# Kernel optimization log

Hardware: AMD Instinct MI355X
Metric: run time of the kernel (lower is better)

## Reference

```python
import jax, jax.numpy as jnp
import numpy as np

EPS = 1e-8  # torch F.cosine_similarity default eps
NEG = -1e9  # masked_fill value


def setup_inputs() -> dict:
    key = jax.random.key(0)
    k1, k2, k3 = jax.random.split(key, 3)
    B, Sq, Sk, D = 4, 2048, 2048, 1024
    query = jax.random.normal(k1, (B, Sq, 1, D), dtype=jnp.float32)
    key_t = jax.random.normal(k2, (B, 1, Sk, D), dtype=jnp.float32)
    mask = jax.random.randint(k3, (B, Sk), 0, 2, dtype=jnp.int32)
    return {"query": query, "key": key_t, "mask": mask}


def reference(query, key, mask):
    # query: [B, Sq, 1, D], key: [B, 1, Sk, D]
    q = query[:, :, 0, :]  # [B, Sq, D]
    k = key[:, 0, :, :]    # [B, Sk, D]
    # cosine_similarity(q, k, dim=3) = (q.k) / (max(|q|,eps) * max(|k|,eps))
    qn = jnp.maximum(jnp.linalg.norm(q, axis=-1), EPS)  # [B, Sq]
    kn = jnp.maximum(jnp.linalg.norm(k, axis=-1), EPS)  # [B, Sk]
    dot = jnp.einsum('bqd,bkd->bqk', q, k)              # [B, Sq, Sk]
    scores = dot / (qn[:, :, None] * kn[:, None, :])
    # mask.unsqueeze(1).repeat(1, Sq, 1) -> broadcast [B, 1, Sk] over Sq
    scores = jnp.where(mask[:, None, :] == 0, NEG, scores)
    return scores
```

## Files before the change

kernel.cpp:

```cpp
#include <hip/hip_runtime.h>
#include <hip/hip_bf16.h>
#include <stdint.h>


constexpr int B_  = 4;
constexpr int SQ  = 2048;
constexpr int SK  = 2048;
constexpr int D_  = 1024;
constexpr int BM  = 128;
constexpr int BN  = 128;
constexpr int BK  = 64;
constexpr int BKf = 32;

typedef __attribute__((ext_vector_type(8))) short    short8;
typedef __attribute__((ext_vector_type(4))) float    f32x4;
typedef __attribute__((ext_vector_type(4))) unsigned uint4v;
typedef unsigned int u32;

__device__ inline unsigned pack_bf16(float lo, float hi) {
  union { float f; unsigned u; } a, b;
  a.f = lo; b.f = hi;
  return __builtin_amdgcn_perm(b.u, a.u, 0x07060302u);
}

__device__ inline void async_ld16(const void* g, void* l) {
  __builtin_amdgcn_global_load_lds((const __attribute__((address_space(1))) u32*)g,
                                   (__attribute__((address_space(3))) u32*)l, 16, 0, 0);
}

constexpr int ROWS_Q = B_ * SQ;
constexpr int ROWS_T = B_ * (SQ + SK);

__global__ __launch_bounds__(256) void convert_norm(
    const float* __restrict__ Q, const float* __restrict__ Km,
    unsigned short* __restrict__ Qb, unsigned short* __restrict__ Kb,
    float* __restrict__ invQ, float* __restrict__ invK)
{
  const int row  = blockIdx.x * 4 + (threadIdx.x >> 6);
  const int lane = threadIdx.x & 63;

  const float* src; unsigned short* dst; float* inv;
  if (row < ROWS_Q) {
    src = Q  + (size_t)row * D_;
    dst = Qb + (size_t)row * D_;
    inv = invQ + row;
  } else {
    int r = row - ROWS_Q;
    src = Km + (size_t)r * D_;
    dst = Kb + (size_t)r * D_;
    inv = invK + r;
  }

  const f32x4* s4 = (const f32x4*)(src + lane * 16);
  f32x4 v[4];
  #pragma unroll
  for (int i = 0; i < 4; ++i) v[i] = s4[i];

  float ss = 0.0f;
  unsigned p[8];
  #pragma unroll
  for (int i = 0; i < 4; ++i) {
    p[2*i]   = pack_bf16(v[i].x, v[i].y);
    p[2*i+1] = pack_bf16(v[i].z, v[i].w);
    ss += v[i].x*v[i].x + v[i].y*v[i].y + v[i].z*v[i].z + v[i].w*v[i].w;
  }
  uint4v w0 = {p[0], p[1], p[2], p[3]};
  uint4v w1 = {p[4], p[5], p[6], p[7]};
  uint4v* d4 = (uint4v*)(dst + lane * 16);
  d4[0] = w0; d4[1] = w1;

  #pragma unroll
  for (int off = 32; off > 0; off >>= 1) ss += __shfl_xor(ss, off);
  if (lane == 0) *inv = 1.0f / fmaxf(sqrtf(ss), 1e-8f);
}

__global__ __launch_bounds__(256, 2) void ca_gemm_bf(
    const unsigned short* __restrict__ Qb,
    const unsigned short* __restrict__ Kb,
    const float* __restrict__ invQ,
    const float* __restrict__ invK,
    const int*   __restrict__ mask,
    float*       __restrict__ out)
{
  __shared__ __align__(16) unsigned short As[BM * BK];
  __shared__ __align__(16) unsigned short Bs[BN * BK];

  const int tid  = threadIdx.x;
  const int lane = tid & 63;
  const int w    = tid >> 6;
  const int b    = blockIdx.z;
  const int tm0  = blockIdx.y * BM;
  const int tn0  = blockIdx.x * BN;

  const int srow   = lane >> 3;
  const int gchunk = (lane & 7) ^ srow;

  const char* qrow = (const char*)(Qb + ((size_t)b * SQ + tm0 + w * 32 + srow) * D_) + gchunk * 16;
  const char* krow = (const char*)(Kb + ((size_t)b * SK + tn0 + w * 32 + srow) * D_) + gchunk * 16;
  const size_t rstep8 = (size_t)8 * D_ * 2;

  unsigned short* ldsA = &As[(size_t)(w * 32) * BK];
  unsigned short* ldsB = &Bs[(size_t)(w * 32) * BK];

  f32x4 zero4 = {0.0f, 0.0f, 0.0f, 0.0f};
  f32x4 acc[4][4];
  #pragma unroll
  for (int i = 0; i < 4; ++i)
    #pragma unroll
    for (int j = 0; j < 4; ++j) acc[i][j] = zero4;

  const int wm = (w >> 1) * 64;
  const int wn = (w & 1) * 64;
  const int lr = lane & 15;
  const int lq = lane >> 4;

  for (int k0 = 0; k0 < D_; k0 += BK) {
    __syncthreads();
    const size_t kb = (size_t)k0 * 2;
    #pragma unroll
    for (int i = 0; i < 4; ++i)
      async_ld16(qrow + kb + i * rstep8, ldsA + i * 8 * BK);
    #pragma unroll
    for (int i = 0; i < 4; ++i)
      async_ld16(krow + kb + i * rstep8, ldsB + i * 8 * BK);
    __syncthreads();

    #pragma unroll
    for (int s = 0; s < 2; ++s) {
      short8 af[4], bf[4];
      #pragma unroll
      for (int t = 0; t < 4; ++t) {
        const int r = wm + t * 16 + lr;
        af[t] = *(const short8*)&As[(size_t)r * BK + (size_t)(((s * 4 + lq) ^ (r & 7)) * 8)];
      }
      #pragma unroll
      for (int t = 0; t < 4; ++t) {
        const int r = wn + t * 16 + lr;
        bf[t] = *(const short8*)&Bs[(size_t)r * BK + (size_t)(((s * 4 + lq) ^ (r & 7)) * 8)];
      }
      #pragma unroll
      for (int i = 0; i < 4; ++i)
        #pragma unroll
        for (int j = 0; j < 4; ++j)
          acc[i][j] = __builtin_amdgcn_mfma_f32_16x16x32_bf16(af[i], bf[j], acc[i][j], 0, 0, 0);
    }
  }

  #pragma unroll
  for (int tn = 0; tn < 4; ++tn) {
    const int gc = tn0 + wn + tn * 16 + lr;
    const int mk = mask[b * SK + gc];
    const float ib = invK[b * SK + gc];
    #pragma unroll
    for (int tm = 0; tm < 4; ++tm) {
      const int lrow = wm + tm * 16 + lq * 4;
      #pragma unroll
      for (int r = 0; r < 4; ++r) {
        const float ia = invQ[b * SQ + tm0 + lrow + r];
        float v = mk ? acc[tm][tn][r] * ia * ib : -1000000000.0f;
        out[((size_t)b * SQ + tm0 + lrow + r) * SK + gc] = v;
      }
    }
  }
}

constexpr int LDK = 40;

__global__ __launch_bounds__(256, 2) void ca_gemm(
    const float* __restrict__ Q, const float* __restrict__ Km,
    const int* __restrict__ mask, float* __restrict__ out)
{
  __shared__ __align__(16) short As[BM * LDK];
  __shared__ __align__(16) short Bs[BN * LDK];
  __shared__ float ssA_part[256];
  __shared__ float ssB_part[256];
  __shared__ float invA[BM];
  __shared__ float invB[BN];

  const int tid  = threadIdx.x;
  const int lane = tid & 63;
  const int w    = tid >> 6;
  const int b    = blockIdx.z;
  const int tm0  = blockIdx.y * BM;
  const int tn0  = blockIdx.x * BN;

  const int ra = tid >> 1;
  const int ka = (tid & 1) * 16;

  const float* qp = Q  + ((size_t)b * SQ + tm0 + ra) * D_ + ka;
  const float* kp = Km + ((size_t)b * SK + tn0 + ra) * D_ + ka;

  f32x4 zero4 = {0.0f, 0.0f, 0.0f, 0.0f};
  f32x4 acc[4][4];
  #pragma unroll
  for (int i = 0; i < 4; ++i)
    #pragma unroll
    for (int j = 0; j < 4; ++j) acc[i][j] = zero4;

  float ssA = 0.0f, ssB = 0.0f;

  const int wm = (w >> 1) * 64;
  const int wn = (w & 1) * 64;
  const int lr = lane & 15;
  const int lq = lane >> 4;

  short* aw = &As[ra * LDK + ka];
  short* bw = &Bs[ra * LDK + ka];

  for (int k0 = 0; k0 < D_; k0 += BKf) {
    f32x4 av[4], bv[4];
    #pragma unroll
    for (int i = 0; i < 4; ++i) av[i] = *(const f32x4*)(qp + 4 * i);
    #pragma unroll
    for (int i = 0; i < 4; ++i) bv[i] = *(const f32x4*)(kp + 4 * i);
    qp += BKf; kp += BKf;

    unsigned pa[8], pb[8];
    #pragma unroll
    for (int i = 0; i < 4; ++i) {
      pa[2*i]   = pack_bf16(av[i].x, av[i].y);
      pa[2*i+1] = pack_bf16(av[i].z, av[i].w);
      pb[2*i]   = pack_bf16(bv[i].x, bv[i].y);
      pb[2*i+1] = pack_bf16(bv[i].z, bv[i].w);
      ssA += av[i].x*av[i].x + av[i].y*av[i].y + av[i].z*av[i].z + av[i].w*av[i].w;
      ssB += bv[i].x*bv[i].x + bv[i].y*bv[i].y + bv[i].z*bv[i].z + bv[i].w*bv[i].w;
    }

    __syncthreads();
    {
      uint4v wa0 = {pa[0], pa[1], pa[2], pa[3]};
      uint4v wa1 = {pa[4], pa[5], pa[6], pa[7]};
      uint4v wb0 = {pb[0], pb[1], pb[2], pb[3]};
      uint4v wb1 = {pb[4], pb[5], pb[6], pb[7]};
      *(uint4v*)(aw)     = wa0;
      *(uint4v*)(aw + 8) = wa1;
      *(uint4v*)(bw)     = wb0;
      *(uint4v*)(bw + 8) = wb1;
    }
    __syncthreads();

    short8 af[4], bf[4];
    #pragma unroll
    for (int t = 0; t < 4; ++t)
      af[t] = *(const short8*)&As[(wm + t * 16 + lr) * LDK + lq * 8];
    #pragma unroll
    for (int t = 0; t < 4; ++t)
      bf[t] = *(const short8*)&Bs[(wn + t * 16 + lr) * LDK + lq * 8];

    #pragma unroll
    for (int i = 0; i < 4; ++i)
      #pragma unroll
      for (int j = 0; j < 4; ++j)
        acc[i][j] = __builtin_amdgcn_mfma_f32_16x16x32_bf16(af[i], bf[j], acc[i][j], 0, 0, 0);
  }

  ssA_part[tid] = ssA;
  ssB_part[tid] = ssB;
  __syncthreads();
  if (tid < BM) {
    float s = ssA_part[2 * tid] + ssA_part[2 * tid + 1];
    invA[tid] = 1.0f / fmaxf(sqrtf(s), 1e-8f);
  } else {
    int r = tid - BM;
    float s = ssB_part[2 * r] + ssB_part[2 * r + 1];
    invB[r] = 1.0f / fmaxf(sqrtf(s), 1e-8f);
  }
  __syncthreads();

  #pragma unroll
  for (int tn = 0; tn < 4; ++tn) {
    const int lc = wn + tn * 16 + lr;
    const int gc = tn0 + lc;
    const int mk = mask[b * SK + gc];
    const float ib = invB[lc];
    #pragma unroll
    for (int tm = 0; tm < 4; ++tm) {
      const int lrow = wm + tm * 16 + lq * 4;
      #pragma unroll
      for (int r = 0; r < 4; ++r) {
        float v = mk ? acc[tm][tn][r] * invA[lrow + r] * ib : -1000000000.0f;
        out[((size_t)b * SQ + tm0 + lrow + r) * SK + gc] = v;
      }
    }
  }
}

extern "C" void kernel_launch(void* const* d_in, const int* in_sizes, int n_in,
                              void* d_out, int out_size, void* d_ws, size_t ws_size,
                              hipStream_t stream) {
  const float* Q    = (const float*)d_in[0];
  const float* Km   = (const float*)d_in[1];
  const int*   mask = (const int*)d_in[2];
  float*       out  = (float*)d_out;

  const size_t nQ   = (size_t)B_ * SQ * D_;
  const size_t nK   = (size_t)B_ * SK * D_;
  const size_t need = (nQ + nK) * 2 + (size_t)B_ * (SQ + SK) * 4;
  if (ws_size >= need) {
    unsigned short* Qb = (unsigned short*)d_ws;
    unsigned short* Kb = Qb + nQ;
    float*          iQ = (float*)(Kb + nK);
    float*          iK = iQ + (size_t)B_ * SQ;
    convert_norm<<<ROWS_T / 4, 256, 0, stream>>>(Q, Km, Qb, Kb, iQ, iK);
    dim3 grid(SK / BN, SQ / BM, B_);
    ca_gemm_bf<<<grid, dim3(256), 0, stream>>>(Qb, Kb, iQ, iK, mask, out);
  } else {
    dim3 grid(SK / BN, SQ / BM, B_);
    ca_gemm<<<grid, dim3(256), 0, stream>>>(Q, Km, mask, out);
  }
}
```

Measured before the change: 161.7 us.

## Double-buffer LDS tiles in bf16 GEMM with async prefetch and nontemporal stores

After: 169.9 us. 5.0% more time.

```diff
diff --git a/kernel.cpp b/kernel.cpp
--- a/kernel.cpp
+++ b/kernel.cpp
@@ -9,8 +9,8 @@
 constexpr int D_  = 1024;
 constexpr int BM  = 128;
 constexpr int BN  = 128;
-constexpr int BK  = 64;
-constexpr int BKf = 32;
+constexpr int BK  = 32;
+constexpr int NIT = D_ / BK;
 
 typedef __attribute__((ext_vector_type(8))) short    short8;
 typedef __attribute__((ext_vector_type(4))) float    f32x4;
@@ -82,8 +82,8 @@
     const int*   __restrict__ mask,
     float*       __restrict__ out)
 {
-  __shared__ __align__(16) unsigned short As[BM * BK];
-  __shared__ __align__(16) unsigned short Bs[BN * BK];
+  __shared__ __align__(16) unsigned short As[2][BM * BK];
+  __shared__ __align__(16) unsigned short Bs[2][BN * BK];
 
   const int tid  = threadIdx.x;
   const int lane = tid & 63;
@@ -92,15 +92,15 @@
   const int tm0  = blockIdx.y * BM;
   const int tn0  = blockIdx.x * BN;
 
-  const int srow   = lane >> 3;
-  const int gchunk = (lane & 7) ^ srow;
+  const int srow   = lane >> 2;
+  const int gchunk = (lane & 3) ^ ((lane >> 3) & 3);
 
   const char* qrow = (const char*)(Qb + ((size_t)b * SQ + tm0 + w * 32 + srow) * D_) + gchunk * 16;
   const char* krow = (const char*)(Kb + ((size_t)b * SK + tn0 + w * 32 + srow) * D_) + gchunk * 16;
-  const size_t rstep8 = (size_t)8 * D_ * 2;
-
-  unsigned short* ldsA = &As[(size_t)(w * 32) * BK];
-  unsigned short* ldsB = &Bs[(size_t)(w * 32) * BK];
+  const size_t rstep16 = (size_t)16 * D_ * 2;
+
+  unsigned short* ldsA0[2] = { &As[0][(w * 32) * BK], &As[1][(w * 32) * BK] };
+  unsigned short* ldsB0[2] = { &Bs[0][(w * 32) * BK], &Bs[1][(w * 32) * BK] };
 
   f32x4 zero4 = {0.0f, 0.0f, 0.0f, 0.0f};
   f32x4 acc[4][4];
@@ -114,51 +114,67 @@
   const int lr = lane & 15;
   const int lq = lane >> 4;
 
-  for (int k0 = 0; k0 < D_; k0 += BK) {
-    __syncthreads();
-    const size_t kb = (size_t)k0 * 2;
-    #pragma unroll
-    for (int i = 0; i < 4; ++i)
-      async_ld16(qrow + kb + i * rstep8, ldsA + i * 8 * BK);
-    #pragma unroll
-    for (int i = 0; i < 4; ++i)
-      async_ld16(krow + kb + i * rstep8, ldsB + i * 8 * BK);
-    __syncthreads();
-
-    #pragma unroll
-    for (int s = 0; s < 2; ++s) {
-      short8 af[4], bf[4];
-      #pragma unroll
-      for (int t = 0; t < 4; ++t) {
-        const int r = wm + t * 16 + lr;
-        af[t] = *(const short8*)&As[(size_t)r * BK + (size_t)(((s * 4 + lq) ^ (r & 7)) * 8)];
-      }
-      #pragma unroll
-      for (int t = 0; t < 4; ++t) {
-        const int r = wn + t * 16 + lr;
-        bf[t] = *(const short8*)&Bs[(size_t)r * BK + (size_t)(((s * 4 + lq) ^ (r & 7)) * 8)];
-      }
-      #pragma unroll
-      for (int i = 0; i < 4; ++i)
-        #pragma unroll
-        for (int j = 0; j < 4; ++j)
-          acc[i][j] = __builtin_amdgcn_mfma_f32_16x16x32_bf16(af[i], bf[j], acc[i][j], 0, 0, 0);
-    }
-  }
-
+  int   mk[4]; float ib[4]; float ia[4][4];
   #pragma unroll
   for (int tn = 0; tn < 4; ++tn) {
     const int gc = tn0 + wn + tn * 16 + lr;
-    const int mk = mask[b * SK + gc];
-    const float ib = invK[b * SK + gc];
+    mk[tn] = mask[b * SK + gc];
+    ib[tn] = invK[b * SK + gc];
+  }
+  #pragma unroll
+  for (int tm = 0; tm < 4; ++tm) {
+    const int lrow = wm + tm * 16 + lq * 4;
+    #pragma unroll
+    for (int r = 0; r < 4; ++r) ia[tm][r] = invQ[b * SQ + tm0 + lrow + r];
+  }
+
+  auto stage = [&](int buf, int k0) {
+    const size_t kb = (size_t)k0 * 2;
+    async_ld16(qrow + kb,           ldsA0[buf]);
+    async_ld16(qrow + kb + rstep16, ldsA0[buf] + 16 * BK);
+    async_ld16(krow + kb,           ldsB0[buf]);
+    async_ld16(krow + kb + rstep16, ldsB0[buf] + 16 * BK);
+  };
+
+  auto compute = [&](const unsigned short* Ac, const unsigned short* Bc) {
+    short8 af[4], bf[4];
+    #pragma unroll
+    for (int t = 0; t < 4; ++t) {
+      const int r = wm + t * 16 + lr;
+      af[t] = *(const short8*)&Ac[(size_t)r * BK + (size_t)((lq ^ ((r >> 1) & 3)) * 8)];
+    }
+    #pragma unroll
+    for (int t = 0; t < 4; ++t) {
+      const int r = wn + t * 16 + lr;
+      bf[t] = *(const short8*)&Bc[(size_t)r * BK + (size_t)((lq ^ ((r >> 1) & 3)) * 8)];
+    }
+    #pragma unroll
+    for (int i = 0; i < 4; ++i)
+      #pragma unroll
+      for (int j = 0; j < 4; ++j)
+        acc[i][j] = __builtin_amdgcn_mfma_f32_16x16x32_bf16(af[i], bf[j], acc[i][j], 0, 0, 0);
+  };
+
+  stage(0, 0);
+  for (int it = 0; it < NIT; it += 2) {
+    __syncthreads();
+    if (it + 1 < NIT) stage(1, (it + 1) * BK);
+    compute(As[0], Bs[0]);
+    __syncthreads();
+    if (it + 2 < NIT) stage(0, (it + 2) * BK);
+    compute(As[1], Bs[1]);
+  }
+
+  #pragma unroll
+  for (int tn = 0; tn < 4; ++tn) {
+    const int gc = tn0 + wn + tn * 16 + lr;
     #pragma unroll
     for (int tm = 0; tm < 4; ++tm) {
       const int lrow = wm + tm * 16 + lq * 4;
       #pragma unroll
       for (int r = 0; r < 4; ++r) {
-        const float ia = invQ[b * SQ + tm0 + lrow + r];
-        float v = mk ? acc[tm][tn][r] * ia * ib : -1000000000.0f;
-        out[((size_t)b * SQ + tm0 + lrow + r) * SK + gc] = v;
+        float v = mk[tn] ? acc[tm][tn][r] * ia[tm][r] * ib[tn] : -1000000000.0f;
+        __builtin_nontemporal_store(v, &out[((size_t)b * SQ + tm0 + lrow + r) * SK + gc]);
       }
     }
   }
@@ -207,13 +223,13 @@
   short* aw = &As[ra * LDK + ka];
   short* bw = &Bs[ra * LDK + ka];
 
-  for (int k0 = 0; k0 < D_; k0 += BKf) {
+  for (int k0 = 0; k0 < D_; k0 += 32) {
     f32x4 av[4], bv[4];
     #pragma unroll
     for (int i = 0; i < 4; ++i) av[i] = *(const f32x4*)(qp + 4 * i);
     #pragma unroll
     for (int i = 0; i < 4; ++i) bv[i] = *(const f32x4*)(kp + 4 * i);
-    qp += BKf; kp += BKf;
+    qp += 32; kp += 32;
 
     unsigned pa[8], pb[8];
     #pragma unroll
@@ -272,13 +288,13 @@
     const int lc = wn + tn * 16 + lr;
     const int gc = tn0 + lc;
     const int mk = mask[b * SK + gc];
-    const float ib = invB[lc];
+    const float ibv = invB[lc];
     #pragma unroll
     for (int tm = 0; tm < 4; ++tm) {
       const int lrow = wm + tm * 16 + lq * 4;
       #pragma unroll
       for (int r = 0; r < 4; ++r) {
-        float v = mk ? acc[tm][tn][r] * invA[lrow + r] * ib : -1000000000.0f;
+        float v = mk ? acc[tm][tn][r] * invA[lrow + r] * ibv : -1000000000.0f;
         out[((size_t)b * SQ + tm0 + lrow + r) * SK + gc] = v;
       }
     }
```
